# Kernel optimization log

Measured on AMD Instinct MI355X. Metric: run time of the kernel, lower is better.

Reference implementation:

```python
import jax, jax.numpy as jnp
import numpy as np

B, N, DIM, H, DH = 4, 4096, 1024, 16, 64
INNER = H * DH


def setup_inputs() -> dict:
    key = jax.random.key(0)
    k1, k2, k3, k4 = jax.random.split(key, 4)
    x = jax.random.normal(k1, (B, N, DIM), dtype=jnp.float32)
    mask = jax.random.randint(k2, (B, N), 0, 2).astype(bool)
    Wqkv = jax.random.normal(k3, (DIM, 3 * INNER), dtype=jnp.float32) * (DIM ** -0.5)
    Wout = jax.random.normal(k4, (INNER, DIM), dtype=jnp.float32) * (INNER ** -0.5)
    bout = jnp.zeros((DIM,), dtype=jnp.float32)
    return {"x": x, "mask": mask, "Wqkv": Wqkv, "Wout": Wout, "bout": bout}


def _split_heads(t):
    b, n, _ = t.shape
    return t.reshape(b, n, H, DH).transpose(0, 2, 1, 3)  # b h n d


def reference(x, mask, Wqkv, Wout, bout):
    qkv = x @ Wqkv                      # [b, n, 3*inner]
    q, k, v = jnp.split(qkv, 3, axis=-1)
    q, k, v = map(_split_heads, (q, k, v))  # [b, h, n, d]
    q = jax.nn.elu(q) + 1.0
    k = jax.nn.elu(k) + 1.0
    m = mask[:, None, :, None]          # [b, 1, n, 1]
    k = jnp.where(m, k, 0.0)
    v = jnp.where(m, v, 0.0)
    kv = jnp.einsum('bhnd,bhne->bhde', k, v)      # [b, h, d, d]
    out = jnp.einsum('bhnd,bhde->bhne', q, kv)    # [b, h, n, d]
    z = 1.0 / (jnp.einsum('bhnd,bhd->bhn', q, k.sum(axis=2)) + 1e-6)
    out = out * z[..., None]
    out = out.transpose(0, 2, 1, 3).reshape(x.shape[0], -1, INNER)  # [b, n, inner]
    return out @ Wout + bout
```

## Files before the change

kernel.cpp:

```cpp
#include <hip/hip_runtime.h>
#include <hip/hip_bf16.h>
#include <cstddef>
#include <cstdint>

#define B_     4
#define N_     4096
#define DIM_   1024
#define H_     16
#define DH_    64
#define INNER_ 1024
#define MTOK   (B_ * N_)
#define QKVC   (3 * INNER_)
#define NCH    16
#define CHUNK  (N_ / NCH)

typedef __attribute__((ext_vector_type(8))) short short8;
typedef __attribute__((ext_vector_type(4))) float f32x4;

__device__ __forceinline__ float elu1(float x) {
    return x > 0.f ? x + 1.f : __expf(x);
}
__device__ __forceinline__ unsigned short f2bf(float f) {
    __hip_bfloat16 h = __float2bfloat16(f);
    return __builtin_bit_cast(unsigned short, h);
}
__device__ __forceinline__ float bf2f(unsigned short u) {
    __hip_bfloat16 h = __builtin_bit_cast(__hip_bfloat16, u);
    return __bfloat162float(h);
}

__device__ __forceinline__ void gload16(const void* g, void* l) {
    __builtin_amdgcn_global_load_lds(
        (const __attribute__((address_space(1))) unsigned int*)g,
        (__attribute__((address_space(3))) unsigned int*)l, 16, 0, 0);
}

__global__ __launch_bounds__(256) void prep_fused(
    const float* __restrict__ x, unsigned short* __restrict__ xbf,
    const float* __restrict__ Wqkv, unsigned short* __restrict__ wqkvT,
    const float* __restrict__ Wout, unsigned short* __restrict__ woutT)
{
    __shared__ float t[32][33];
    const int blk = blockIdx.x;
    if (blk < 2048) {
        const long n8 = (long)MTOK * DIM_ / 8;
        const long stride = 2048L * 256;
        for (long i = (long)blk * 256 + threadIdx.x; i < n8; i += stride) {
            const float4 f0 = reinterpret_cast<const float4*>(x)[2 * i];
            const float4 f1 = reinterpret_cast<const float4*>(x)[2 * i + 1];
            short8 u;
            u[0] = (short)f2bf(f0.x); u[1] = (short)f2bf(f0.y);
            u[2] = (short)f2bf(f0.z); u[3] = (short)f2bf(f0.w);
            u[4] = (short)f2bf(f1.x); u[5] = (short)f2bf(f1.y);
            u[6] = (short)f2bf(f1.z); u[7] = (short)f2bf(f1.w);
            reinterpret_cast<short8*>(xbf)[i] = u;
        }
        return;
    }
    const float* src; unsigned short* dst; int R, C, r0, c0;
    if (blk < 5120) {
        const int id = blk - 2048;
        src = Wqkv; dst = wqkvT; R = DIM_; C = QKVC;
        r0 = (id & 31) * 32; c0 = (id >> 5) * 32;
    } else {
        const int id = blk - 5120;
        src = Wout; dst = woutT; R = INNER_; C = INNER_;
        r0 = (id & 31) * 32; c0 = (id >> 5) * 32;
    }
    const int tx = threadIdx.x & 31, ty = threadIdx.x >> 5;
#pragma unroll
    for (int i = 0; i < 4; ++i)
        t[ty * 4 + i][tx] = src[(size_t)(r0 + ty * 4 + i) * C + c0 + tx];
    __syncthreads();
#pragma unroll
    for (int i = 0; i < 4; ++i)
        dst[(size_t)(c0 + ty * 4 + i) * R + r0 + tx] = f2bf(t[tx][ty * 4 + i]);
}

template<int EPI, int HAS_BIAS>
__global__ __launch_bounds__(512, 2) void gemm256(
    const unsigned short* __restrict__ A,
    const unsigned short* __restrict__ BT,
    void* __restrict__ Cv,
    unsigned short* __restrict__ Ckv,
    const float* __restrict__ bias,
    const int* __restrict__ msk,
    int M, int N, int K, int lda, int ldb, int ldc)
{
    __shared__ __align__(16) unsigned short smem[4][256 * 64];

    const int tid = threadIdx.x;
    const int wv  = tid >> 6;
    const int ln  = tid & 63;
    const int wr  = wv >> 2;
    const int wc  = wv & 3;

    const int nwg = gridDim.x;
    int wg = blockIdx.x;
    {
        const int q = nwg >> 3, r = nwg & 7;
        const int xcd = wg & 7, lid = wg >> 3;
        wg = (xcd < r ? xcd * (q + 1) : r * (q + 1) + (xcd - r) * q) + lid;
    }
    const int ncol = N >> 8;
    const int bx = wg % ncol;
    const int by = wg / ncol;
    const int row0 = by << 8;
    const int col0 = bx << 8;

    const int l8    = ln >> 3;
    const int sslot = ((ln & 7) ^ l8) << 3;

    const int lr16 = ln & 15;
    const int kc   = ln >> 4;
    const int sw   = lr16 & 7;
    const int soff0 = (kc ^ sw) << 3;
    const int soff1 = ((4 + kc) ^ sw) << 3;

    f32x4 acc[8][4];
#pragma unroll
    for (int m = 0; m < 8; ++m)
#pragma unroll
        for (int n = 0; n < 4; ++n) acc[m][n] = f32x4{0.f, 0.f, 0.f, 0.f};

    const int NT = K >> 6;

#pragma unroll
    for (int i = 0; i < 4; ++i) {
        const int lr = wv * 32 + i * 8;
        gload16(&A [(size_t)(row0 + lr + l8) * lda + sslot], &smem[0][lr * 64]);
        gload16(&BT[(size_t)(col0 + lr + l8) * ldb + sslot], &smem[2][lr * 64]);
    }
    __syncthreads();

    for (int t = 0; t < NT; ++t) {
        const int cur = t & 1;
        const unsigned short* bufA = smem[cur];
        const unsigned short* bufB = smem[2 + cur];
        short8 bf[4][2];
        short8 af[2][2][2];

#pragma unroll
        for (int n = 0; n < 4; ++n) {
            const int row = wc * 64 + n * 16 + lr16;
            bf[n][0] = *reinterpret_cast<const short8*>(&bufB[row * 64 + soff0]);
            bf[n][1] = *reinterpret_cast<const short8*>(&bufB[row * 64 + soff1]);
        }
#pragma unroll
        for (int mi = 0; mi < 2; ++mi) {
            const int row = wr * 128 + mi * 16 + lr16;
            af[0][mi][0] = *reinterpret_cast<const short8*>(&bufA[row * 64 + soff0]);
            af[0][mi][1] = *reinterpret_cast<const short8*>(&bufA[row * 64 + soff1]);
        }
        if (t + 1 < NT) {
            const int k0 = (t + 1) << 6;
            unsigned short* nA = smem[cur ^ 1];
            unsigned short* nB = smem[2 + (cur ^ 1)];
#pragma unroll
            for (int i = 0; i < 4; ++i) {
                const int lr = wv * 32 + i * 8;
                gload16(&A [(size_t)(row0 + lr + l8) * lda + k0 + sslot],
                        &nA[lr * 64]);
                gload16(&BT[(size_t)(col0 + lr + l8) * ldb + k0 + sslot],
                        &nB[lr * 64]);
            }
        }

#pragma unroll
        for (int p = 0; p < 4; ++p) {
            if (p > 0) __builtin_amdgcn_s_barrier();
            if (p < 3) {
#pragma unroll
                for (int mi = 0; mi < 2; ++mi) {
                    const int row = wr * 128 + ((p + 1) * 2 + mi) * 16 + lr16;
                    af[(p + 1) & 1][mi][0] =
                        *reinterpret_cast<const short8*>(&bufA[row * 64 + soff0]);
                    af[(p + 1) & 1][mi][1] =
                        *reinterpret_cast<const short8*>(&bufA[row * 64 + soff1]);
                }
            }
            __builtin_amdgcn_s_setprio(1);
#pragma unroll
            for (int mi = 0; mi < 2; ++mi)
#pragma unroll
                for (int n = 0; n < 4; ++n) {
                    acc[p * 2 + mi][n] = __builtin_amdgcn_mfma_f32_16x16x32_bf16(
                        af[p & 1][mi][0], bf[n][0], acc[p * 2 + mi][n], 0, 0, 0);
                    acc[p * 2 + mi][n] = __builtin_amdgcn_mfma_f32_16x16x32_bf16(
                        af[p & 1][mi][1], bf[n][1], acc[p * 2 + mi][n], 0, 0, 0);
                }
            __builtin_amdgcn_s_setprio(0);
        }
        __syncthreads();
    }

    const int orow = (ln >> 4) << 2;
    const int ocol = ln & 15;

    const bool kvpath = (EPI == 2) || (EPI == 3 && col0 >= 1024);

    if (kvpath) {
        unsigned short* tb = &smem[0][0];
        const int kvbase = (EPI == 3) ? 1024 : 0;
        const int klimit = (EPI == 3) ? 2048 : 1024;
#pragma unroll
        for (int m = 0; m < 8; ++m) {
            const int rrb = wr * 128 + m * 16 + orow;
            const int4 m4 = *reinterpret_cast<const int4*>(&msk[row0 + rrb]);
            int mv[4] = { m4.x, m4.y, m4.z, m4.w };
            const int slot16 = rrb >> 3, half = (rrb >> 2) & 1;
#pragma unroll
            for (int n = 0; n < 4; ++n) {
                const int chl = wc * 64 + n * 16 + ocol;
                const bool isk = (col0 + chl) < klimit;
                ushort4 st;
#pragma unroll
                for (int r2 = 0; r2 < 4; ++r2) {
                    float o = acc[m][n][r2];
                    o = mv[r2] ? (isk ? elu1(o) : o) : 0.f;
                    ((unsigned short*)&st)[r2] = f2bf(o);
                }
                *reinterpret_cast<ushort4*>(
                    &tb[chl * 256 + ((slot16 ^ (chl & 7)) << 3) + half * 4]) = st;
            }
        }
        __syncthreads();
        unsigned short* dst = (EPI == 3) ? Ckv : (unsigned short*)Cv;
        const int ldt = (EPI == 3) ? MTOK : ldc;
#pragma unroll
        for (int i = 0; i < 16; ++i) {
            const int idx = i * 512 + tid;
            const int ch = idx >> 5;
            const int sl = idx & 31;
            const short8 v = *reinterpret_cast<const short8*>(
                &tb[ch * 256 + ((sl ^ (ch & 7)) << 3)]);
            *reinterpret_cast<short8*>(
                &dst[(size_t)(col0 - kvbase + ch) * ldt + row0 + sl * 8]) = v;
        }
    } else {
#pragma unroll
        for (int m = 0; m < 8; ++m) {
            const int rrb = row0 + wr * 128 + m * 16 + orow;
#pragma unroll
            for (int n = 0; n < 4; ++n) {
                const int c = col0 + wc * 64 + n * 16 + ocol;
                float bv = 0.f;
                if constexpr (HAS_BIAS) bv = bias[c];
#pragma unroll
                for (int r2 = 0; r2 < 4; ++r2) {
                    const int rr = rrb + r2;
                    float o = acc[m][n][r2] + bv;
                    if constexpr (EPI == 1 || EPI == 3) {
                        o = elu1(o);
                        ((unsigned short*)Cv)[(size_t)rr * ldc + c] = f2bf(o);
                    } else {
                        ((float*)Cv)[(size_t)rr * ldc + c] = o;
                    }
                }
            }
        }
    }
}

__global__ __launch_bounds__(256) void kv_partial(
    const unsigned short* __restrict__ kvT, float* __restrict__ part)
{
    const int bh = blockIdx.x;
    const int ch = blockIdx.y;
    const int b = bh / H_, h = bh % H_;
    const int tok0 = b * N_ + ch * CHUNK;

    __shared__ __align__(16) unsigned short kt[64 * 64];
    __shared__ __align__(16) unsigned short vt[64 * 64];
    __shared__ float ksr[4][64];

    const int tid = threadIdx.x;
    const int wv = tid >> 6, ln = tid & 63;
    const int wr = wv >> 1, wc = wv & 1;
    const int l8 = ln >> 3;
    const int sslot = ((ln & 7) ^ l8) << 3;
    const int lr16 = ln & 15;
    const int kc = ln >> 4;
    const int sw = lr16 & 7;

    const size_t krow = (size_t)(h * 64) * MTOK;
    const size_t vrow = (size_t)(1024 + h * 64) * MTOK;

    f32x4 acc[2][2];
#pragma unroll
    for (int i = 0; i < 2; ++i)
#pragma unroll
        for (int j = 0; j < 2; ++j) acc[i][j] = f32x4{0.f, 0.f, 0.f, 0.f};

    const int kd = tid & 63, kq = tid >> 6;
    float ksacc = 0.f;

    for (int st = 0; st < 4; ++st) {
        const int tb = tok0 + st * 64;
        __syncthreads();
#pragma unroll
        for (int i = 0; i < 2; ++i) {
            const int rb = (wv * 2 + i) * 8;
            gload16(&kvT[krow + (size_t)(rb + l8) * MTOK + tb + sslot], &kt[rb * 64]);
            gload16(&kvT[vrow + (size_t)(rb + l8) * MTOK + tb + sslot], &vt[rb * 64]);
        }
        __syncthreads();
#pragma unroll
        for (int ks = 0; ks < 2; ++ks) {
            const int soff = ((ks * 4 + kc) ^ sw) << 3;
            short8 af[2], bf[2];
#pragma unroll
            for (int mi = 0; mi < 2; ++mi)
                af[mi] = *reinterpret_cast<const short8*>(
                    &kt[(wr * 32 + mi * 16 + lr16) * 64 + soff]);
#pragma unroll
            for (int ni = 0; ni < 2; ++ni)
                bf[ni] = *reinterpret_cast<const short8*>(
                    &vt[(wc * 32 + ni * 16 + lr16) * 64 + soff]);
#pragma unroll
            for (int mi = 0; mi < 2; ++mi)
#pragma unroll
                for (int ni = 0; ni < 2; ++ni)
                    acc[mi][ni] = __builtin_amdgcn_mfma_f32_16x16x32_bf16(
                        af[mi], bf[ni], acc[mi][ni], 0, 0, 0);
        }
#pragma unroll
        for (int sl = 0; sl < 2; ++sl) {
            const int phys = (kq * 2 + sl) ^ (kd & 7);
            short8 v = *reinterpret_cast<const short8*>(&kt[kd * 64 + phys * 8]);
#pragma unroll
            for (int e = 0; e < 8; ++e) ksacc += bf2f((unsigned short)v[e]);
        }
    }
    ksr[kq][kd] = ksacc;
    __syncthreads();

    float* p = part + ((size_t)bh * NCH + ch) * 4160;
    const int orow = (ln >> 4) << 2;
    const int ocol = ln & 15;
#pragma unroll
    for (int mi = 0; mi < 2; ++mi)
#pragma unroll
        for (int ni = 0; ni < 2; ++ni) {
            const int d0 = wr * 32 + mi * 16 + orow;
            const int e  = wc * 32 + ni * 16 + ocol;
#pragma unroll
            for (int r = 0; r < 4; ++r)
                p[(d0 + r) * 64 + e] = acc[mi][ni][r];
        }
    if (tid < 64)
        p[4096 + tid] = ksr[0][tid] + ksr[1][tid] + ksr[2][tid] + ksr[3][tid];
}

__global__ __launch_bounds__(256) void kv_reduce(
    const float* __restrict__ part, unsigned short* __restrict__ kvtb,
    float* __restrict__ ksumf)
{
    const int bh = blockIdx.x;
    for (int idx = threadIdx.x; idx < 4096; idx += 256) {
        float s = 0.f;
        for (int c = 0; c < NCH; ++c)
            s += part[((size_t)bh * NCH + c) * 4160 + idx];
        const int d = idx >> 6, e = idx & 63;
        const unsigned short hi = f2bf(s);
        const float lo = s - bf2f(hi);
        kvtb[(size_t)bh * 8192 + e * 64 + d] = hi;
        kvtb[(size_t)bh * 8192 + 4096 + e * 64 + d] = f2bf(lo);
    }
    if (threadIdx.x < 64) {
        float s = 0.f;
        for (int c = 0; c < NCH; ++c)
            s += part[((size_t)bh * NCH + c) * 4160 + 4096 + threadIdx.x];
        ksumf[bh * 64 + threadIdx.x] = s;
    }
}

__global__ __launch_bounds__(256) void attn_mfma(
    const unsigned short* __restrict__ qbf,
    const unsigned short* __restrict__ kvtb,
    const float* __restrict__ ksumf,
    unsigned short* __restrict__ attnbf)
{
    const int bh = blockIdx.x, tt = blockIdx.y;
    const int b = bh / H_, h = bh % H_;
    const int tok0 = b * N_ + tt * 256;

    __shared__ __align__(16) unsigned short qt[256 * 64];
    __shared__ float den[256];

    const int tid = threadIdx.x;
    const int wv = tid >> 6, ln = tid & 63;
    const int l8 = ln >> 3;
    const int sslot = ((ln & 7) ^ l8) << 3;
    const int lr16 = ln & 15;
    const int kc = ln >> 4;

    const unsigned short* kvb = kvtb + (size_t)bh * 8192;
    short8 bhf[4][2], blf[4][2];
#pragma unroll
    for (int n = 0; n < 4; ++n)
#pragma unroll
        for (int ks = 0; ks < 2; ++ks) {
            const int off = (n * 16 + lr16) * 64 + ks * 32 + kc * 8;
            bhf[n][ks] = *reinterpret_cast<const short8*>(&kvb[off]);
            blf[n][ks] = *reinterpret_cast<const short8*>(&kvb[4096 + off]);
        }

#pragma unroll
    for (int i = 0; i < 8; ++i) {
        const int rb = wv * 64 + i * 8;
        gload16(&qbf[(size_t)(tok0 + rb + l8) * INNER_ + h * 64 + sslot],
                &qt[rb * 64]);
    }

    {
        float dsum = 0.f;
        const unsigned short* qr = &qbf[(size_t)(tok0 + tid) * INNER_ + h * 64];
        const float* ksp = &ksumf[bh * 64];
#pragma unroll
        for (int j = 0; j < 8; ++j) {
            short8 v = *reinterpret_cast<const short8*>(&qr[j * 8]);
#pragma unroll
            for (int e = 0; e < 8; ++e)
                dsum += bf2f((unsigned short)v[e]) * ksp[j * 8 + e];
        }
        den[tid] = dsum;
    }
    __syncthreads();

    f32x4 acc[4][4];
#pragma unroll
    for (int m = 0; m < 4; ++m)
#pragma unroll
        for (int n = 0; n < 4; ++n) acc[m][n] = f32x4{0.f, 0.f, 0.f, 0.f};

#pragma unroll
    for (int ks = 0; ks < 2; ++ks) {
        const int soff = ((ks * 4 + kc) ^ (lr16 & 7)) << 3;
        short8 af[4];
#pragma unroll
        for (int m = 0; m < 4; ++m)
            af[m] = *reinterpret_cast<const short8*>(
                &qt[(wv * 64 + m * 16 + lr16) * 64 + soff]);
#pragma unroll
        for (int m = 0; m < 4; ++m)
#pragma unroll
            for (int n = 0; n < 4; ++n) {
                acc[m][n] = __builtin_amdgcn_mfma_f32_16x16x32_bf16(
                    af[m], bhf[n][ks], acc[m][n], 0, 0, 0);
                acc[m][n] = __builtin_amdgcn_mfma_f32_16x16x32_bf16(
                    af[m], blf[n][ks], acc[m][n], 0, 0, 0);
            }
    }

    const int orow = (ln >> 4) << 2;
    const int ocol = ln & 15;
#pragma unroll
    for (int m = 0; m < 4; ++m) {
        const int rl = wv * 64 + m * 16 + orow;
#pragma unroll
        for (int r = 0; r < 4; ++r) {
            const float z = 1.f / (den[rl + r] + 1e-6f);
            const size_t orow_g = (size_t)(tok0 + rl + r) * INNER_ + h * 64;
#pragma unroll
            for (int n = 0; n < 4; ++n)
                attnbf[orow_g + n * 16 + ocol] = f2bf(acc[m][n][r] * z);
        }
    }
}

extern "C" void kernel_launch(void* const* d_in, const int* in_sizes, int n_in,
                              void* d_out, int out_size, void* d_ws, size_t ws_size,
                              hipStream_t stream)
{
    const float* x    = (const float*)d_in[0];
    const int*   mask = (const int*)d_in[1];
    const float* Wqkv = (const float*)d_in[2];
    const float* Wout = (const float*)d_in[3];
    const float* bout = (const float*)d_in[4];
    float* out = (float*)d_out;

    const size_t need = 127156224;
    if (ws_size < need) return;

    char* base = (char*)d_ws;
    unsigned short* xbf    = (unsigned short*)base;
    unsigned short* attnbf = xbf;
    unsigned short* kvT    = (unsigned short*)(base + 33554432);
    unsigned short* wqkvT  = (unsigned short*)(base + 100663296);
    unsigned short* woutT  = (unsigned short*)(base + 106954752);
    float* part  = (float*)(base + 109051904);
    unsigned short* kvtb = (unsigned short*)(base + 126091264);
    float* ksumf = (float*)(base + 127139840);
    unsigned short* qbf = (unsigned short*)d_out;

    prep_fused<<<dim3(6144), dim3(256), 0, stream>>>(
        x, xbf, Wqkv, wqkvT, Wout, woutT);

    gemm256<3, 0><<<dim3(64 * 12), dim3(512), 0, stream>>>(
        xbf, wqkvT, qbf, kvT, nullptr, mask,
        MTOK, QKVC, DIM_, DIM_, DIM_, 1024);

    kv_partial<<<dim3(B_ * H_, NCH), dim3(256), 0, stream>>>(kvT, part);
    kv_reduce<<<dim3(B_ * H_), dim3(256), 0, stream>>>(part, kvtb, ksumf);

    attn_mfma<<<dim3(B_ * H_, N_ / 256), dim3(256), 0, stream>>>(
        qbf, kvtb, ksumf, attnbf);

    gemm256<0, 1><<<dim3(64 * 4), dim3(512), 0, stream>>>(
        attnbf, woutT, out, nullptr, bout, nullptr,
        MTOK, INNER_, INNER_, INNER_, INNER_, INNER_);
}
```

Baseline: 235.6 us.

## Fuse fp32-to-bf16 conversion of x into the QKV GEMM A-tile load

Drops the separate pass that converts x to bf16 in the prep kernel. The QKV GEMM now reads fp32 x directly, converting it to bf16 in registers and writing it to the swizzled LDS layout. The next tile's loads are issued early and stored after the MFMA phase. This removes one full read and write of the 64MB activation through HBM. In exchange, x is re-read in fp32 by each of the 12 column tiles, and the A loads no longer use async global-to-LDS copies, which raises register pressure and VALU work in the main loop.

```diff
diff --git a/kernel.cpp b/kernel.cpp
--- a/kernel.cpp
+++ b/kernel.cpp
@@ -35,35 +35,18 @@
         (__attribute__((address_space(3))) unsigned int*)l, 16, 0, 0);
 }
 
-__global__ __launch_bounds__(256) void prep_fused(
-    const float* __restrict__ x, unsigned short* __restrict__ xbf,
+__global__ __launch_bounds__(256) void prep_w(
     const float* __restrict__ Wqkv, unsigned short* __restrict__ wqkvT,
     const float* __restrict__ Wout, unsigned short* __restrict__ woutT)
 {
     __shared__ float t[32][33];
     const int blk = blockIdx.x;
-    if (blk < 2048) {
-        const long n8 = (long)MTOK * DIM_ / 8;
-        const long stride = 2048L * 256;
-        for (long i = (long)blk * 256 + threadIdx.x; i < n8; i += stride) {
-            const float4 f0 = reinterpret_cast<const float4*>(x)[2 * i];
-            const float4 f1 = reinterpret_cast<const float4*>(x)[2 * i + 1];
-            short8 u;
-            u[0] = (short)f2bf(f0.x); u[1] = (short)f2bf(f0.y);
-            u[2] = (short)f2bf(f0.z); u[3] = (short)f2bf(f0.w);
-            u[4] = (short)f2bf(f1.x); u[5] = (short)f2bf(f1.y);
-            u[6] = (short)f2bf(f1.z); u[7] = (short)f2bf(f1.w);
-            reinterpret_cast<short8*>(xbf)[i] = u;
-        }
-        return;
-    }
     const float* src; unsigned short* dst; int R, C, r0, c0;
-    if (blk < 5120) {
-        const int id = blk - 2048;
+    if (blk < 3072) {
         src = Wqkv; dst = wqkvT; R = DIM_; C = QKVC;
-        r0 = (id & 31) * 32; c0 = (id >> 5) * 32;
+        r0 = (blk & 31) * 32; c0 = (blk >> 5) * 32;
     } else {
-        const int id = blk - 5120;
+        const int id = blk - 3072;
         src = Wout; dst = woutT; R = INNER_; C = INNER_;
         r0 = (id & 31) * 32; c0 = (id >> 5) * 32;
     }
@@ -77,9 +60,9 @@
         dst[(size_t)(c0 + ty * 4 + i) * R + r0 + tx] = f2bf(t[tx][ty * 4 + i]);
 }
 
-template<int EPI, int HAS_BIAS>
+template<int EPI, int HAS_BIAS, int AF32>
 __global__ __launch_bounds__(512, 2) void gemm256(
-    const unsigned short* __restrict__ A,
+    const void* __restrict__ Av,
     const unsigned short* __restrict__ BT,
     void* __restrict__ Cv,
     unsigned short* __restrict__ Ckv,
@@ -87,6 +70,9 @@
     const int* __restrict__ msk,
     int M, int N, int K, int lda, int ldb, int ldc)
 {
+    const unsigned short* A  = (const unsigned short*)Av;
+    const float*          Af = (const float*)Av;
+
     __shared__ __align__(16) unsigned short smem[4][256 * 64];
 
     const int tid = threadIdx.x;
@@ -125,10 +111,30 @@
 
     const int NT = K >> 6;
 
+    if constexpr (AF32) {
+#pragma unroll
+        for (int i = 0; i < 4; ++i) {
+            const int lr = wv * 32 + i * 8;
+            const float* s = &Af[(size_t)(row0 + lr + l8) * lda + sslot];
+            const float4 a0 = *reinterpret_cast<const float4*>(s);
+            const float4 a1 = *reinterpret_cast<const float4*>(s + 4);
+            short8 u;
+            u[0] = (short)f2bf(a0.x); u[1] = (short)f2bf(a0.y);
+            u[2] = (short)f2bf(a0.z); u[3] = (short)f2bf(a0.w);
+            u[4] = (short)f2bf(a1.x); u[5] = (short)f2bf(a1.y);
+            u[6] = (short)f2bf(a1.z); u[7] = (short)f2bf(a1.w);
+            *reinterpret_cast<short8*>(&smem[0][lr * 64 + ln * 8]) = u;
+        }
+    } else {
+#pragma unroll
+        for (int i = 0; i < 4; ++i) {
+            const int lr = wv * 32 + i * 8;
+            gload16(&A[(size_t)(row0 + lr + l8) * lda + sslot], &smem[0][lr * 64]);
+        }
+    }
 #pragma unroll
     for (int i = 0; i < 4; ++i) {
         const int lr = wv * 32 + i * 8;
-        gload16(&A [(size_t)(row0 + lr + l8) * lda + sslot], &smem[0][lr * 64]);
         gload16(&BT[(size_t)(col0 + lr + l8) * ldb + sslot], &smem[2][lr * 64]);
     }
     __syncthreads();
@@ -139,7 +145,18 @@
         const unsigned short* bufB = smem[2 + cur];
         short8 bf[4][2];
         short8 af[2][2][2];
-
+        float4 ar[4][2];
+
+        if (AF32 && t + 1 < NT) {
+            const int k0 = (t + 1) << 6;
+#pragma unroll
+            for (int i = 0; i < 4; ++i) {
+                const int lr = wv * 32 + i * 8;
+                const float* s = &Af[(size_t)(row0 + lr + l8) * lda + k0 + sslot];
+                ar[i][0] = *reinterpret_cast<const float4*>(s);
+                ar[i][1] = *reinterpret_cast<const float4*>(s + 4);
+            }
+        }
 #pragma unroll
         for (int n = 0; n < 4; ++n) {
             const int row = wc * 64 + n * 16 + lr16;
@@ -159,8 +176,9 @@
 #pragma unroll
             for (int i = 0; i < 4; ++i) {
                 const int lr = wv * 32 + i * 8;
-                gload16(&A [(size_t)(row0 + lr + l8) * lda + k0 + sslot],
-                        &nA[lr * 64]);
+                if constexpr (!AF32)
+                    gload16(&A[(size_t)(row0 + lr + l8) * lda + k0 + sslot],
+                            &nA[lr * 64]);
                 gload16(&BT[(size_t)(col0 + lr + l8) * ldb + k0 + sslot],
                         &nB[lr * 64]);
             }
@@ -191,18 +209,29 @@
                 }
             __builtin_amdgcn_s_setprio(0);
         }
+        if (AF32 && t + 1 < NT) {
+            unsigned short* nA = smem[cur ^ 1];
+#pragma unroll
+            for (int i = 0; i < 4; ++i) {
+                const int lr = wv * 32 + i * 8;
+                short8 u;
+                u[0] = (short)f2bf(ar[i][0].x); u[1] = (short)f2bf(ar[i][0].y);
+                u[2] = (short)f2bf(ar[i][0].z); u[3] = (short)f2bf(ar[i][0].w);
+                u[4] = (short)f2bf(ar[i][1].x); u[5] = (short)f2bf(ar[i][1].y);
+                u[6] = (short)f2bf(ar[i][1].z); u[7] = (short)f2bf(ar[i][1].w);
+                *reinterpret_cast<short8*>(&nA[lr * 64 + ln * 8]) = u;
+            }
+        }
         __syncthreads();
     }
 
     const int orow = (ln >> 4) << 2;
     const int ocol = ln & 15;
 
-    const bool kvpath = (EPI == 2) || (EPI == 3 && col0 >= 1024);
+    const bool kvpath = (EPI == 3 && col0 >= 1024);
 
     if (kvpath) {
         unsigned short* tb = &smem[0][0];
-        const int kvbase = (EPI == 3) ? 1024 : 0;
-        const int klimit = (EPI == 3) ? 2048 : 1024;
 #pragma unroll
         for (int m = 0; m < 8; ++m) {
             const int rrb = wr * 128 + m * 16 + orow;
@@ -212,7 +241,7 @@
 #pragma unroll
             for (int n = 0; n < 4; ++n) {
                 const int chl = wc * 64 + n * 16 + ocol;
-                const bool isk = (col0 + chl) < klimit;
+                const bool isk = (col0 + chl) < 2048;
                 ushort4 st;
 #pragma unroll
                 for (int r2 = 0; r2 < 4; ++r2) {
@@ -225,8 +254,6 @@
             }
         }
         __syncthreads();
-        unsigned short* dst = (EPI == 3) ? Ckv : (unsigned short*)Cv;
-        const int ldt = (EPI == 3) ? MTOK : ldc;
 #pragma unroll
         for (int i = 0; i < 16; ++i) {
             const int idx = i * 512 + tid;
@@ -235,7 +262,7 @@
             const short8 v = *reinterpret_cast<const short8*>(
                 &tb[ch * 256 + ((sl ^ (ch & 7)) << 3)]);
             *reinterpret_cast<short8*>(
-                &dst[(size_t)(col0 - kvbase + ch) * ldt + row0 + sl * 8]) = v;
+                &Ckv[(size_t)(col0 - 1024 + ch) * MTOK + row0 + sl * 8]) = v;
         }
     } else {
 #pragma unroll
@@ -484,8 +511,7 @@
     if (ws_size < need) return;
 
     char* base = (char*)d_ws;
-    unsigned short* xbf    = (unsigned short*)base;
-    unsigned short* attnbf = xbf;
+    unsigned short* attnbf = (unsigned short*)base;
     unsigned short* kvT    = (unsigned short*)(base + 33554432);
     unsigned short* wqkvT  = (unsigned short*)(base + 100663296);
     unsigned short* woutT  = (unsigned short*)(base + 106954752);
@@ -494,11 +520,10 @@
     float* ksumf = (float*)(base + 127139840);
     unsigned short* qbf = (unsigned short*)d_out;
 
-    prep_fused<<<dim3(6144), dim3(256), 0, stream>>>(
-        x, xbf, Wqkv, wqkvT, Wout, woutT);
-
-    gemm256<3, 0><<<dim3(64 * 12), dim3(512), 0, stream>>>(
-        xbf, wqkvT, qbf, kvT, nullptr, mask,
+    prep_w<<<dim3(4096), dim3(256), 0, stream>>>(Wqkv, wqkvT, Wout, woutT);
+
+    gemm256<3, 0, 1><<<dim3(64 * 12), dim3(512), 0, stream>>>(
+        x, wqkvT, qbf, kvT, nullptr, mask,
         MTOK, QKVC, DIM_, DIM_, DIM_, 1024);
 
     kv_partial<<<dim3(B_ * H_, NCH), dim3(256), 0, stream>>>(kvT, part);
@@ -507,7 +532,7 @@
     attn_mfma<<<dim3(B_ * H_, N_ / 256), dim3(256), 0, stream>>>(
         qbf, kvtb, ksumf, attnbf);
 
-    gemm256<0, 1><<<dim3(64 * 4), dim3(512), 0, stream>>>(
+    gemm256<0, 1, 0><<<dim3(64 * 4), dim3(512), 0, stream>>>(
         attnbf, woutT, out, nullptr, bout, nullptr,
         MTOK, INNER_, INNER_, INNER_, INNER_, INNER_);
 }
```

New measurement: 294.6 us. +25.1%, slower.
